# Optimization experiments

Measured on AMD Instinct MI355X. Metric: run time of the kernel, lower is better.

Reference implementation:

```python
import jax, jax.numpy as jnp
import numpy as np

N, E, D, L = 50000, 625000, 128, 7
EPS = 1e-7   # GENConv message epsilon
T = 1.0      # softmax aggregation temperature (learn_t=False)
NUM_ATOM_FEATS, ATOM_VOCAB = 9, 64
NUM_BOND_FEATS, BOND_VOCAB = 3, 8


def setup_inputs() -> dict:
    key = jax.random.key(0)
    ks = jax.random.split(key, 9)
    x = jax.random.randint(ks[0], (N, NUM_ATOM_FEATS), 0, ATOM_VOCAB, dtype=jnp.int32)
    edge_index = jax.random.randint(ks[1], (2, E), 0, N, dtype=jnp.int32)
    edge_attr = jax.random.randint(ks[2], (E, NUM_BOND_FEATS), 0, BOND_VOCAB, dtype=jnp.int32)
    atom_emb = jax.random.normal(ks[3], (NUM_ATOM_FEATS, ATOM_VOCAB, D), dtype=jnp.float32) * 0.1
    bond_emb = jax.random.normal(ks[4], (NUM_BOND_FEATS, BOND_VOCAB, D), dtype=jnp.float32) * 0.1
    W = jax.random.normal(ks[5], (L, D, D), dtype=jnp.float32) / np.sqrt(D).astype(np.float32)
    b = jnp.zeros((L, D), dtype=jnp.float32)
    ln_gamma = jnp.ones((L, D), dtype=jnp.float32)
    ln_beta = jnp.zeros((L, D), dtype=jnp.float32)
    return dict(x=x, edge_index=edge_index, edge_attr=edge_attr,
                atom_emb=atom_emb, bond_emb=bond_emb, W=W, b=b,
                ln_gamma=ln_gamma, ln_beta=ln_beta)


def _layer_norm(h, g, bta):
    mu = jnp.mean(h, axis=-1, keepdims=True)
    var = jnp.var(h, axis=-1, keepdims=True)
    return (h - mu) * jax.lax.rsqrt(var + 1e-5) * g + bta


def _gen_conv(h, src, dst, edge_emb, Wl, bl):
    # GENConv: msg = relu(x_j + e) + eps; softmax aggregation over dst; Linear(x + m)
    msg = jax.nn.relu(h[src] + edge_emb) + EPS                 # [E, D]
    logits = msg * T
    seg_max = jax.ops.segment_max(logits, dst, num_segments=N)  # [N, D]
    seg_max = jnp.where(jnp.isfinite(seg_max), seg_max, 0.0)    # empty segments
    e = jnp.exp(logits - seg_max[dst])                          # [E, D]
    denom = jax.ops.segment_sum(e, dst, num_segments=N)         # [N, D]
    alpha = e / (denom[dst] + 1e-16)
    m = jax.ops.segment_sum(alpha * msg, dst, num_segments=N)   # [N, D]
    return (h + m) @ Wl + bl


def reference(x, edge_index, edge_attr, atom_emb, bond_emb, W, b, ln_gamma, ln_beta):
    src, dst = edge_index[0], edge_index[1]
    # AtomEncoder: sum of per-feature embedding lookups -> [N, D]
    h = jnp.sum(atom_emb[jnp.arange(NUM_ATOM_FEATS)[None, :], x], axis=1)
    # BondEncoder (conv_encode_edge=False: encoded once) -> [E, D]
    edge_emb = jnp.sum(bond_emb[jnp.arange(NUM_BOND_FEATS)[None, :], edge_attr], axis=1)
    # res+ block, dropout=0 (no-op)
    h = _gen_conv(h, src, dst, edge_emb, W[0], b[0])
    for layer in range(1, L):
        h2 = jax.nn.relu(_layer_norm(h, ln_gamma[layer - 1], ln_beta[layer - 1]))
        h = _gen_conv(h2, src, dst, edge_emb, W[layer], b[layer]) + h
    h = _layer_norm(h, ln_gamma[L - 1], ln_beta[L - 1])
    return h
```

## Files before the change

### kernel.cpp

```cpp
#include <hip/hip_runtime.h>
#include <hip/hip_fp16.h>
#include <math.h>


constexpr int D = 128;
constexpr int NA = 9;
constexpr int NB = 3;
constexpr float L2E = 1.4426950408889634f;
constexpr float INV_L2E = 0.6931471805599453f;

using half8  = __attribute__((ext_vector_type(8))) _Float16;
using h2v    = __attribute__((ext_vector_type(2))) _Float16;
using floatx4 = __attribute__((ext_vector_type(4))) float;


__global__ void k_hist(const int* __restrict__ dst, int* __restrict__ deg, int E) {
    int e = blockIdx.x * 256 + threadIdx.x;
    if (e < E) atomicAdd(&deg[dst[e]], 1);
}

__global__ void k_scan_a(const int* __restrict__ deg, int* __restrict__ offs,
                         int* __restrict__ bsum, int N) {
    __shared__ int s[256];
    int i = blockIdx.x * 256 + threadIdx.x;
    int v = (i < N) ? deg[i] : 0;
    s[threadIdx.x] = v;
    __syncthreads();
    for (int d = 1; d < 256; d <<= 1) {
        int add = (threadIdx.x >= d) ? s[threadIdx.x - d] : 0;
        __syncthreads();
        s[threadIdx.x] += add;
        __syncthreads();
    }
    if (i < N) offs[i + 1] = s[threadIdx.x];
    if (threadIdx.x == 255) bsum[blockIdx.x] = s[255];
    if (i == 0) offs[0] = 0;
}

__global__ void k_scan_b(const int* __restrict__ bsum, int* __restrict__ bexc, int nb) {
    __shared__ int s[256];
    int t = threadIdx.x;
    int v = (t < nb) ? bsum[t] : 0;
    s[t] = v;
    __syncthreads();
    for (int d = 1; d < 256; d <<= 1) {
        int add = (t >= d) ? s[t - d] : 0;
        __syncthreads();
        s[t] += add;
        __syncthreads();
    }
    if (t < nb) bexc[t] = s[t] - v;
}

__global__ void k_scan_c_dhist(int* __restrict__ offs, const int* __restrict__ bexc,
                               const int* __restrict__ deg, int* __restrict__ dbin,
                               int N) {
    __shared__ int lb[64];
    int t = threadIdx.x;
    if (t < 64) lb[t] = 0;
    __syncthreads();
    int i = blockIdx.x * 256 + t;
    if (i < N) {
        offs[i + 1] += bexc[blockIdx.x];
        int d = deg[i]; d = d < 63 ? d : 63;
        atomicAdd(&lb[63 - d], 1);
    }
    __syncthreads();
    if (t < 64 && lb[t] > 0) atomicAdd(&dbin[t], lb[t]);
}

__global__ void k_fill(const int* __restrict__ src, const int* __restrict__ dst,
                       const int* __restrict__ attr, const int* __restrict__ offs,
                       int* __restrict__ cur, unsigned* __restrict__ recs1,
                       const int* __restrict__ dbin, int* __restrict__ doff, int E) {
    int e = blockIdx.x * 256 + threadIdx.x;
    if (e < E) {
        int d = dst[e];
        int pos = offs[d] + atomicAdd(&cur[d], 1);
        unsigned cidx = (unsigned)(attr[e * 3] * 64 + attr[e * 3 + 1] * 8 + attr[e * 3 + 2]);
        recs1[pos] = (unsigned)src[e] | (cidx << 17);
    }
    if (blockIdx.x == 0 && threadIdx.x == 0) {
        int acc = 0;
        for (int b = 0; b < 64; ++b) { doff[b] = acc; acc += dbin[b]; }
    }
}


__global__ void k_dfill(const int* __restrict__ deg, const int* __restrict__ doff,
                        int* __restrict__ dcur, int* __restrict__ perm, int N) {
    __shared__ int lc[64], lbase[64];
    int t = threadIdx.x;
    if (t < 64) lc[t] = 0;
    __syncthreads();
    int i = blockIdx.x * 256 + t;
    int b = 0, rank = 0;
    if (i < N) {
        int d = deg[i]; d = d < 63 ? d : 63;
        b = 63 - d;
        rank = atomicAdd(&lc[b], 1);
    }
    __syncthreads();
    if (t < 64 && lc[t] > 0) lbase[t] = atomicAdd(&dcur[t], lc[t]);
    __syncthreads();
    if (i < N) perm[doff[b] + lbase[b] + rank] = i;
}

__global__ void k_comb(const float* __restrict__ bemb, __half* __restrict__ comb16,
                       int* __restrict__ deg, int* __restrict__ cur,
                       int* __restrict__ dbin, int* __restrict__ dcur, int N) {
    int gid = blockIdx.x * 256 + threadIdx.x;
    if (gid < N) { deg[gid] = 0; cur[gid] = 0; }
    if (gid < 64) { dbin[gid] = 0; dcur[gid] = 0; }
    if (gid >= 512 * 32) return;
    int c = gid >> 5, q = gid & 31;
    int a0 = c >> 6, a1 = (c >> 3) & 7, a2 = c & 7;
    float4 v0 = *(const float4*)(bemb + (a0)*D + q * 4);
    float4 v1 = *(const float4*)(bemb + (8 + a1) * D + q * 4);
    float4 v2 = *(const float4*)(bemb + (16 + a2) * D + q * 4);
    __half2* c2 = (__half2*)comb16;
    c2[c * 64 + q * 2]     = __floats2half2_rn(L2E * (v0.x + v1.x + v2.x),
                                               L2E * (v0.y + v1.y + v2.y));
    c2[c * 64 + q * 2 + 1] = __floats2half2_rn(L2E * (v0.z + v1.z + v2.z),
                                               L2E * (v0.w + v1.w + v2.w));
}

__global__ void k_wt(const float* __restrict__ W, __half* __restrict__ Wt16, int total) {
    int o = blockIdx.x * 256 + threadIdx.x;
    if (o >= total) return;
    int l = o >> 14;
    int rem = o & 16383;
    int f = rem >> 7, k = rem & 127;
    Wt16[o] = __float2half_rn(W[(l << 14) + k * 128 + f]);
}


__global__ void k_atom(const int* __restrict__ x, const float* __restrict__ aemb,
                       __half* __restrict__ h16, int N) {
    int wid = (blockIdx.x * blockDim.x + threadIdx.x) >> 6;
    int lane = threadIdx.x & 63;
    if (wid >= N) return;
    const int* xr = x + wid * NA;
    float ax = 0.f, ay = 0.f;
#pragma unroll
    for (int f = 0; f < NA; ++f) {
        int v = xr[f];
        const float2 e = *(const float2*)(aemb + (f * 64 + v) * D + 2 * lane);
        ax += e.x; ay += e.y;
    }
    ((__half2*)h16)[wid * 64 + lane] = __floats2half2_rn(ax * L2E, ay * L2E);
}


__global__ __launch_bounds__(256) void k_agg(const __half* __restrict__ h16,
                      const unsigned* __restrict__ recs1,
                      const int* __restrict__ offs, const __half* __restrict__ comb16,
                      const int* __restrict__ perm,
                      __half* __restrict__ t16, int N) {
    int wid = (blockIdx.x * blockDim.x + threadIdx.x) >> 6;
    int lane = threadIdx.x & 63;
    if (wid >= N) return;
    int nid = perm[wid];
    int su = __builtin_amdgcn_readfirstlane(offs[nid]);
    int eu = __builtin_amdgcn_readfirstlane(offs[nid + 1]);
    h2v hm2 = ((const h2v*)h16)[nid * 64 + lane];
    float hsx = (float)hm2[0], hsy = (float)hm2[1];
    if (su >= eu) {
        ((__half2*)t16)[nid * 64 + lane] =
            __floats2half2_rn(hsx * INV_L2E, hsy * INV_L2E);
        return;
    }
    float Sx = 0.f, Sy = 0.f, Wx = 0.f, Wy = 0.f;

    const h2v* hrow = (const h2v*)h16 + lane;
    const h2v* crow = (const h2v*)comb16 + lane;
    const h2v zero2 = (h2v)(_Float16)0;

    h2v hq[16], cq[16];

    int e0 = su;
    do {
        int lastc = (eu < e0 + 64) ? eu : e0 + 64;
        int last = lastc - 1;
        int ridx = e0 + lane;
        ridx = (ridx < eu - 1) ? ridx : eu - 1;
        unsigned recv = recs1[ridx];

        auto load4 = [&](int base, int slot) {
#pragma unroll
            for (int i = 0; i < 4; ++i) {
                int idx = base + i; idx = (idx < last) ? idx : last;
                unsigned r = __builtin_amdgcn_readlane(recv, idx - e0);
                int sj = (int)(r & 0x1FFFFu);
                int cj = (int)(r >> 17);
                hq[slot * 4 + i] = hrow[sj * 64];
                cq[slot * 4 + i] = crow[cj * 64];
            }
        };
        auto comp4u = [&](int slot) {
#pragma unroll
            for (int i = 0; i < 4; ++i) {
                h2v m = hq[slot * 4 + i] + cq[slot * 4 + i];
                m = __builtin_elementwise_max(m, zero2);
                float u0 = (float)m[0], u1 = (float)m[1];
                float px = __builtin_amdgcn_exp2f(u0);
                float py = __builtin_amdgcn_exp2f(u1);
                Sx += px; Sy += py;
                Wx = fmaf(px, u0, Wx);
                Wy = fmaf(py, u1, Wy);
            }
        };
        auto comp4m = [&](int gb, int slot) {
#pragma unroll
            for (int i = 0; i < 4; ++i) {
                h2v m = hq[slot * 4 + i] + cq[slot * 4 + i];
                m = __builtin_elementwise_max(m, zero2);
                float u0 = (float)m[0], u1 = (float)m[1];
                bool valid = (gb + i) < eu;
                float px = valid ? __builtin_amdgcn_exp2f(u0) : 0.f;
                float py = valid ? __builtin_amdgcn_exp2f(u1) : 0.f;
                Sx += px; Sy += py;
                Wx = fmaf(px, u0, Wx);
                Wy = fmaf(py, u1, Wy);
            }
        };

        load4(e0, 0);
        if (e0 + 4  < lastc) load4(e0 + 4, 1);
        if (e0 + 8  < lastc) load4(e0 + 8, 2);
        if (e0 + 12 < lastc) load4(e0 + 12, 3);

        int e = e0;
        for (; e + 16 < lastc; e += 16) {
            comp4u(0); comp4u(1); comp4u(2); comp4u(3);
            load4(e + 16, 0); load4(e + 20, 1); load4(e + 24, 2); load4(e + 28, 3);
        }
        comp4m(e, 0);
        if (e + 4  < lastc) comp4m(e + 4, 1);
        if (e + 8  < lastc) comp4m(e + 8, 2);
        if (e + 12 < lastc) comp4m(e + 12, 3);

        e0 = lastc;
    } while (e0 < eu);

    float tx = (hsx + Wx / (Sx + 1e-16f)) * INV_L2E;
    float ty = (hsy + Wy / (Sy + 1e-16f)) * INV_L2E;
    ((__half2*)t16)[nid * 64 + lane] = __floats2half2_rn(tx, ty);
}


template <int MODE>
__global__ __launch_bounds__(256) void k_gemm(const __half* __restrict__ A16,
                                              const __half* __restrict__ Wt16,
                                              const float* __restrict__ bl,
                                              const __half* __restrict__ res16,
                                              __half* __restrict__ hres16,
                                              const float* __restrict__ g,
                                              const float* __restrict__ bta,
                                              __half* __restrict__ h16,
                                              float* __restrict__ out,
                                              int N, int useRes) {
    __shared__ float2 sm[2][2][16];
    int lane = threadIdx.x & 63;
    int wave = threadIdx.x >> 6;
    int grp = wave >> 1, half = wave & 1;
    int quad = lane >> 4, col = lane & 15;
    int node = blockIdx.x * 32 + grp * 16 + col;
    bool nok = node < N;
    int nc = nok ? node : N - 1;

    const __half* arow = A16 + (size_t)nc * 128;
    half8 bfrag[4];
#pragma unroll
    for (int ks = 0; ks < 4; ++ks)
        bfrag[ks] = *(const half8*)(arow + ks * 32 + quad * 8);

    uint2 rr[4];
    if (useRes) {
#pragma unroll
        for (int ft2 = 0; ft2 < 4; ++ft2) {
            int f0 = (half * 4 + ft2) * 16 + quad * 4;
            rr[ft2] = *(const uint2*)(res16 + (size_t)nc * 128 + f0);
        }
    }

    floatx4 acc[4];
#pragma unroll
    for (int ft2 = 0; ft2 < 4; ++ft2) acc[ft2] = (floatx4){0.f, 0.f, 0.f, 0.f};

#pragma unroll
    for (int ft2 = 0; ft2 < 4; ++ft2) {
        const __half* wrow = Wt16 + (size_t)((half * 4 + ft2) * 16 + col) * 128;
#pragma unroll
        for (int ks = 0; ks < 4; ++ks) {
            half8 afrag = *(const half8*)(wrow + ks * 32 + quad * 8);
            acc[ft2] = __builtin_amdgcn_mfma_f32_16x16x32_f16(afrag, bfrag[ks],
                                                              acc[ft2], 0, 0, 0);
        }
    }

    float s = 0.f, ss = 0.f;
#pragma unroll
    for (int ft2 = 0; ft2 < 4; ++ft2) {
        int f0 = (half * 4 + ft2) * 16 + quad * 4;
        float4 bb = *(const float4*)(bl + f0);
        float o0 = acc[ft2][0] + bb.x, o1 = acc[ft2][1] + bb.y;
        float o2 = acc[ft2][2] + bb.z, o3 = acc[ft2][3] + bb.w;
        if (useRes) {
            __half2 r01 = *(__half2*)&rr[ft2].x, r23 = *(__half2*)&rr[ft2].y;
            o0 += __low2float(r01); o1 += __high2float(r01);
            o2 += __low2float(r23); o3 += __high2float(r23);
        }
        acc[ft2][0] = o0; acc[ft2][1] = o1; acc[ft2][2] = o2; acc[ft2][3] = o3;
        s += (o0 + o1) + (o2 + o3);
        ss += fmaf(o0, o0, o1 * o1) + fmaf(o2, o2, o3 * o3);
        if (MODE == 0 && nok) {
            __half2 h01 = __floats2half2_rn(o0, o1);
            __half2 h23 = __floats2half2_rn(o2, o3);
            uint2 pk = make_uint2(*(unsigned*)&h01, *(unsigned*)&h23);
            *(uint2*)(hres16 + (size_t)node * 128 + f0) = pk;
        }
    }
    s += __shfl_xor(s, 16, 64);  ss += __shfl_xor(ss, 16, 64);
    s += __shfl_xor(s, 32, 64);  ss += __shfl_xor(ss, 32, 64);
    if (quad == 0) sm[grp][half][col] = make_float2(s, ss);
    __syncthreads();
    float2 oth = sm[grp][half ^ 1][col];
    float st = s + oth.x, sst = ss + oth.y;
    float mu = st * (1.f / 128.f);
    float var = sst * (1.f / 128.f) - mu * mu;
    float rs = rsqrtf(var + 1e-5f);

#pragma unroll
    for (int ft2 = 0; ft2 < 4; ++ft2) {
        int f0 = (half * 4 + ft2) * 16 + quad * 4;
        float4 gg = *(const float4*)(g + f0);
        float4 bt = *(const float4*)(bta + f0);
        float l0 = (acc[ft2][0] - mu) * rs * gg.x + bt.x;
        float l1 = (acc[ft2][1] - mu) * rs * gg.y + bt.y;
        float l2 = (acc[ft2][2] - mu) * rs * gg.z + bt.z;
        float l3 = (acc[ft2][3] - mu) * rs * gg.w + bt.w;
        if (MODE == 0) {
            l0 = fmaxf(l0, 0.f); l1 = fmaxf(l1, 0.f);
            l2 = fmaxf(l2, 0.f); l3 = fmaxf(l3, 0.f);
            if (nok) {
                __half2 h01 = __floats2half2_rn(l0 * L2E, l1 * L2E);
                __half2 h23 = __floats2half2_rn(l2 * L2E, l3 * L2E);
                uint2 pk = make_uint2(*(unsigned*)&h01, *(unsigned*)&h23);
                *(uint2*)(h16 + (size_t)node * 128 + f0) = pk;
            }
        } else {
            if (nok)
                *(float4*)(out + (size_t)node * 128 + f0) =
                    make_float4(l0, l1, l2, l3);
        }
    }
}


extern "C" void kernel_launch(void* const* d_in, const int* in_sizes, int n_in,
                              void* d_out, int out_size, void* d_ws, size_t ws_size,
                              hipStream_t stream) {
    const int*   x    = (const int*)d_in[0];
    const int*   ei   = (const int*)d_in[1];
    const int*   attr = (const int*)d_in[2];
    const float* aemb = (const float*)d_in[3];
    const float* bemb = (const float*)d_in[4];
    const float* Wf   = (const float*)d_in[5];
    const float* bf   = (const float*)d_in[6];
    const float* gam  = (const float*)d_in[7];
    const float* bet  = (const float*)d_in[8];
    float* out = (float*)d_out;

    const int N = in_sizes[0] / NA;
    const int E = in_sizes[1] / 2;
    const int L = in_sizes[5] / (D * D);

    char* ws = (char*)d_ws;
    size_t o = 0;
    auto carve = [&](size_t bytes) -> void* {
        void* p = (void*)(ws + o);
        o += (bytes + 255) & ~(size_t)255;
        return p;
    };
    __half* hres16 = (__half*)carve((size_t)N * D * 2);
    __half* h16    = (__half*)carve((size_t)N * D * 2);
    __half* t16    = (__half*)carve((size_t)N * D * 2);
    unsigned* recs1 = (unsigned*)carve((size_t)E * 4);
    __half* comb16 = (__half*)carve(512 * D * 2);
    __half* Wt16   = (__half*)carve((size_t)L * D * D * 2);
    int*    deg    = (int*)carve((size_t)N * 4);
    int*    cur    = (int*)carve((size_t)N * 4);
    int*    offs   = (int*)carve((size_t)(N + 1) * 4);
    int*    perm   = (int*)carve((size_t)N * 4);
    int*    dbin   = (int*)carve(256);
    int*    doff   = (int*)carve(256);
    int*    dcur   = (int*)carve(256);
    int*    bsum   = (int*)carve(4096);
    int*    bexc   = (int*)carve(4096);

    const int* src = ei;
    const int* dst = ei + E;

    int ebl = (E + 255) / 256;
    int nbl = (N + 255) / 256;

    k_comb<<<nbl, 256, 0, stream>>>(bemb, comb16, deg, cur, dbin, dcur, N);
    int wtot = L * D * D;
    k_wt<<<(wtot + 255) / 256, 256, 0, stream>>>(Wf, Wt16, wtot);
    k_hist<<<ebl, 256, 0, stream>>>(dst, deg, E);
    k_scan_a<<<nbl, 256, 0, stream>>>(deg, offs, bsum, N);
    k_scan_b<<<1, 256, 0, stream>>>(bsum, bexc, nbl);
    k_scan_c_dhist<<<nbl, 256, 0, stream>>>(offs, bexc, deg, dbin, N);
    k_fill<<<ebl, 256, 0, stream>>>(src, dst, attr, offs, cur, recs1, dbin, doff, E);
    k_dfill<<<nbl, 256, 0, stream>>>(deg, doff, dcur, perm, N);

    int wbl = (N * 64 + 255) / 256;
    k_atom<<<wbl, 256, 0, stream>>>(x, aemb, h16, N);

    int gbl = (N + 31) / 32;
    for (int l = 0; l < L; ++l) {
        k_agg<<<wbl, 256, 0, stream>>>(h16, recs1, offs, comb16, perm, t16, N);
        if (l == L - 1) {
            k_gemm<1><<<gbl, 256, 0, stream>>>(t16, Wt16 + l * D * D, bf + l * D,
                                               hres16, hres16,
                                               gam + l * D, bet + l * D, h16, out,
                                               N, 1);
        } else {
            k_gemm<0><<<gbl, 256, 0, stream>>>(t16, Wt16 + l * D * D, bf + l * D,
                                               hres16, hres16,
                                               gam + l * D, bet + l * D, h16, out,
                                               N, l > 0 ? 1 : 0);
        }
    }
}
```

Before: 585.2 us.

## Process four degree-sorted nodes per wave with packed node metadata

Aggregation now assigns four nodes (consecutive in the degree-sorted order) to each wavefront instead of one. A packed int4 metadata array (edge start, edge end, node id) replaces the separate perm and offs lookups, and the first chunk of edge records for all four nodes is prefetched up front. The compute/load interleave in the inner loop is also reordered so each slot's loads are issued right after its compute. This amortises per-node launch and lookup latency and exposes more memory-level parallelism for low-degree nodes, at the cost of serialising four nodes within a wave and adding an extra padded metadata buffer.

After: 590.2 us. No clear change (+0.8%).

```diff
diff --git a/kernel.cpp b/kernel.cpp
--- a/kernel.cpp
+++ b/kernel.cpp
@@ -88,7 +88,8 @@
 
 
 __global__ void k_dfill(const int* __restrict__ deg, const int* __restrict__ doff,
-                        int* __restrict__ dcur, int* __restrict__ perm, int N) {
+                        int* __restrict__ dcur, const int* __restrict__ offs,
+                        int4* __restrict__ meta, int N) {
     __shared__ int lc[64], lbase[64];
     int t = threadIdx.x;
     if (t < 64) lc[t] = 0;
@@ -103,15 +104,18 @@
     __syncthreads();
     if (t < 64 && lc[t] > 0) lbase[t] = atomicAdd(&dcur[t], lc[t]);
     __syncthreads();
-    if (i < N) perm[doff[b] + lbase[b] + rank] = i;
+    if (i < N)
+        meta[doff[b] + lbase[b] + rank] = make_int4(offs[i], offs[i + 1], i, 0);
 }
 
 __global__ void k_comb(const float* __restrict__ bemb, __half* __restrict__ comb16,
                        int* __restrict__ deg, int* __restrict__ cur,
-                       int* __restrict__ dbin, int* __restrict__ dcur, int N) {
+                       int* __restrict__ dbin, int* __restrict__ dcur,
+                       int4* __restrict__ meta, int N, int N4) {
     int gid = blockIdx.x * 256 + threadIdx.x;
     if (gid < N) { deg[gid] = 0; cur[gid] = 0; }
     if (gid < 64) { dbin[gid] = 0; dcur[gid] = 0; }
+    if (gid >= N && gid < N4) meta[gid] = make_int4(0, 0, -1, 0);
     if (gid >= 512 * 32) return;
     int c = gid >> 5, q = gid & 31;
     int a0 = c >> 6, a1 = (c >> 3) & 7, a2 = c & 7;
@@ -154,98 +158,120 @@
 
 __global__ __launch_bounds__(256) void k_agg(const __half* __restrict__ h16,
                       const unsigned* __restrict__ recs1,
-                      const int* __restrict__ offs, const __half* __restrict__ comb16,
-                      const int* __restrict__ perm,
+                      const int4* __restrict__ meta,
+                      const __half* __restrict__ comb16,
                       __half* __restrict__ t16, int N) {
-    int wid = (blockIdx.x * blockDim.x + threadIdx.x) >> 6;
+    int w = (blockIdx.x * blockDim.x + threadIdx.x) >> 6;
     int lane = threadIdx.x & 63;
-    if (wid >= N) return;
-    int nid = perm[wid];
-    int su = __builtin_amdgcn_readfirstlane(offs[nid]);
-    int eu = __builtin_amdgcn_readfirstlane(offs[nid + 1]);
-    h2v hm2 = ((const h2v*)h16)[nid * 64 + lane];
-    float hsx = (float)hm2[0], hsy = (float)hm2[1];
-    if (su >= eu) {
-        ((__half2*)t16)[nid * 64 + lane] =
-            __floats2half2_rn(hsx * INV_L2E, hsy * INV_L2E);
-        return;
-    }
-    float Sx = 0.f, Sy = 0.f, Wx = 0.f, Wy = 0.f;
+    int base = w * 4;
+    if (base >= N) return;
 
     const h2v* hrow = (const h2v*)h16 + lane;
     const h2v* crow = (const h2v*)comb16 + lane;
     const h2v zero2 = (h2v)(_Float16)0;
 
-    h2v hq[16], cq[16];
-
-    int e0 = su;
-    do {
-        int lastc = (eu < e0 + 64) ? eu : e0 + 64;
-        int last = lastc - 1;
-        int ridx = e0 + lane;
-        ridx = (ridx < eu - 1) ? ridx : eu - 1;
-        unsigned recv = recs1[ridx];
-
-        auto load4 = [&](int base, int slot) {
-#pragma unroll
-            for (int i = 0; i < 4; ++i) {
-                int idx = base + i; idx = (idx < last) ? idx : last;
-                unsigned r = __builtin_amdgcn_readlane(recv, idx - e0);
-                int sj = (int)(r & 0x1FFFFu);
-                int cj = (int)(r >> 17);
-                hq[slot * 4 + i] = hrow[sj * 64];
-                cq[slot * 4 + i] = crow[cj * 64];
+    int4 m0 = meta[base], m1 = meta[base + 1], m2 = meta[base + 2], m3 = meta[base + 3];
+    int su0 = __builtin_amdgcn_readfirstlane(m0.x), eu0 = __builtin_amdgcn_readfirstlane(m0.y), nid0 = __builtin_amdgcn_readfirstlane(m0.z);
+    int su1 = __builtin_amdgcn_readfirstlane(m1.x), eu1 = __builtin_amdgcn_readfirstlane(m1.y), nid1 = __builtin_amdgcn_readfirstlane(m1.z);
+    int su2 = __builtin_amdgcn_readfirstlane(m2.x), eu2 = __builtin_amdgcn_readfirstlane(m2.y), nid2 = __builtin_amdgcn_readfirstlane(m2.z);
+    int su3 = __builtin_amdgcn_readfirstlane(m3.x), eu3 = __builtin_amdgcn_readfirstlane(m3.y), nid3 = __builtin_amdgcn_readfirstlane(m3.z);
+
+    unsigned rv0 = 0, rv1 = 0, rv2 = 0, rv3 = 0;
+    if (su0 < eu0) { int ri = su0 + lane; ri = (ri < eu0 - 1) ? ri : eu0 - 1; rv0 = recs1[ri]; }
+    if (su1 < eu1) { int ri = su1 + lane; ri = (ri < eu1 - 1) ? ri : eu1 - 1; rv1 = recs1[ri]; }
+    if (su2 < eu2) { int ri = su2 + lane; ri = (ri < eu2 - 1) ? ri : eu2 - 1; rv2 = recs1[ri]; }
+    if (su3 < eu3) { int ri = su3 + lane; ri = (ri < eu3 - 1) ? ri : eu3 - 1; rv3 = recs1[ri]; }
+
+    auto process = [&](int su, int eu, int nid, unsigned recv) {
+        if (nid < 0) return;
+        h2v hm2 = hrow[nid * 64];
+        if (su >= eu) {
+            ((__half2*)t16)[nid * 64 + lane] = __floats2half2_rn(
+                (float)hm2[0] * INV_L2E, (float)hm2[1] * INV_L2E);
+            return;
+        }
+        float Sx = 0.f, Sy = 0.f, Wx = 0.f, Wy = 0.f;
+        h2v hq[16], cq[16];
+        int e0 = su;
+        bool first = true;
+        do {
+            int lastc = (eu < e0 + 64) ? eu : e0 + 64;
+            int last = lastc - 1;
+            if (!first) {
+                int ri = e0 + lane;
+                ri = (ri < eu - 1) ? ri : eu - 1;
+                recv = recs1[ri];
             }
-        };
-        auto comp4u = [&](int slot) {
-#pragma unroll
-            for (int i = 0; i < 4; ++i) {
-                h2v m = hq[slot * 4 + i] + cq[slot * 4 + i];
-                m = __builtin_elementwise_max(m, zero2);
-                float u0 = (float)m[0], u1 = (float)m[1];
-                float px = __builtin_amdgcn_exp2f(u0);
-                float py = __builtin_amdgcn_exp2f(u1);
-                Sx += px; Sy += py;
-                Wx = fmaf(px, u0, Wx);
-                Wy = fmaf(py, u1, Wy);
+            first = false;
+
+            auto load4 = [&](int b2, int slot) {
+#pragma unroll
+                for (int i = 0; i < 4; ++i) {
+                    int idx = b2 + i; idx = (idx < last) ? idx : last;
+                    unsigned r = __builtin_amdgcn_readlane(recv, idx - e0);
+                    int sj = (int)(r & 0x1FFFFu);
+                    int cj = (int)(r >> 17);
+                    hq[slot * 4 + i] = hrow[sj * 64];
+                    cq[slot * 4 + i] = crow[cj * 64];
+                }
+            };
+            auto comp4u = [&](int slot) {
+#pragma unroll
+                for (int i = 0; i < 4; ++i) {
+                    h2v m = hq[slot * 4 + i] + cq[slot * 4 + i];
+                    m = __builtin_elementwise_max(m, zero2);
+                    float u0 = (float)m[0], u1 = (float)m[1];
+                    float px = __builtin_amdgcn_exp2f(u0);
+                    float py = __builtin_amdgcn_exp2f(u1);
+                    Sx += px; Sy += py;
+                    Wx = fmaf(px, u0, Wx);
+                    Wy = fmaf(py, u1, Wy);
+                }
+            };
+            auto comp4m = [&](int gb, int slot) {
+#pragma unroll
+                for (int i = 0; i < 4; ++i) {
+                    h2v m = hq[slot * 4 + i] + cq[slot * 4 + i];
+                    m = __builtin_elementwise_max(m, zero2);
+                    float u0 = (float)m[0], u1 = (float)m[1];
+                    bool valid = (gb + i) < eu;
+                    float px = valid ? __builtin_amdgcn_exp2f(u0) : 0.f;
+                    float py = valid ? __builtin_amdgcn_exp2f(u1) : 0.f;
+                    Sx += px; Sy += py;
+                    Wx = fmaf(px, u0, Wx);
+                    Wy = fmaf(py, u1, Wy);
+                }
+            };
+
+            load4(e0, 0);
+            if (e0 + 4  < lastc) load4(e0 + 4, 1);
+            if (e0 + 8  < lastc) load4(e0 + 8, 2);
+            if (e0 + 12 < lastc) load4(e0 + 12, 3);
+
+            int e = e0;
+            for (; e + 16 < lastc; e += 16) {
+                comp4u(0); load4(e + 16, 0);
+                comp4u(1); load4(e + 20, 1);
+                comp4u(2); load4(e + 24, 2);
+                comp4u(3); load4(e + 28, 3);
             }
-        };
-        auto comp4m = [&](int gb, int slot) {
-#pragma unroll
-            for (int i = 0; i < 4; ++i) {
-                h2v m = hq[slot * 4 + i] + cq[slot * 4 + i];
-                m = __builtin_elementwise_max(m, zero2);
-                float u0 = (float)m[0], u1 = (float)m[1];
-                bool valid = (gb + i) < eu;
-                float px = valid ? __builtin_amdgcn_exp2f(u0) : 0.f;
-                float py = valid ? __builtin_amdgcn_exp2f(u1) : 0.f;
-                Sx += px; Sy += py;
-                Wx = fmaf(px, u0, Wx);
-                Wy = fmaf(py, u1, Wy);
-            }
-        };
-
-        load4(e0, 0);
-        if (e0 + 4  < lastc) load4(e0 + 4, 1);
-        if (e0 + 8  < lastc) load4(e0 + 8, 2);
-        if (e0 + 12 < lastc) load4(e0 + 12, 3);
-
-        int e = e0;
-        for (; e + 16 < lastc; e += 16) {
-            comp4u(0); comp4u(1); comp4u(2); comp4u(3);
-            load4(e + 16, 0); load4(e + 20, 1); load4(e + 24, 2); load4(e + 28, 3);
-        }
-        comp4m(e, 0);
-        if (e + 4  < lastc) comp4m(e + 4, 1);
-        if (e + 8  < lastc) comp4m(e + 8, 2);
-        if (e + 12 < lastc) comp4m(e + 12, 3);
-
-        e0 = lastc;
-    } while (e0 < eu);
-
-    float tx = (hsx + Wx / (Sx + 1e-16f)) * INV_L2E;
-    float ty = (hsy + Wy / (Sy + 1e-16f)) * INV_L2E;
-    ((__half2*)t16)[nid * 64 + lane] = __floats2half2_rn(tx, ty);
+            comp4m(e, 0);
+            if (e + 4  < lastc) comp4m(e + 4, 1);
+            if (e + 8  < lastc) comp4m(e + 8, 2);
+            if (e + 12 < lastc) comp4m(e + 12, 3);
+
+            e0 = lastc;
+        } while (e0 < eu);
+
+        float tx = ((float)hm2[0] + Wx / (Sx + 1e-16f)) * INV_L2E;
+        float ty = ((float)hm2[1] + Wy / (Sy + 1e-16f)) * INV_L2E;
+        ((__half2*)t16)[nid * 64 + lane] = __floats2half2_rn(tx, ty);
+    };
+
+    process(su0, eu0, nid0, rv0);
+    process(su1, eu1, nid1, rv1);
+    process(su2, eu2, nid2, rv2);
+    process(su3, eu3, nid3, rv3);
 }
 
 
@@ -375,6 +401,7 @@
     const int N = in_sizes[0] / NA;
     const int E = in_sizes[1] / 2;
     const int L = in_sizes[5] / (D * D);
+    const int N4 = (N + 3) & ~3;
 
     char* ws = (char*)d_ws;
     size_t o = 0;
@@ -392,7 +419,7 @@
     int*    deg    = (int*)carve((size_t)N * 4);
     int*    cur    = (int*)carve((size_t)N * 4);
     int*    offs   = (int*)carve((size_t)(N + 1) * 4);
-    int*    perm   = (int*)carve((size_t)N * 4);
+    int4*   meta   = (int4*)carve((size_t)N4 * 16);
     int*    dbin   = (int*)carve(256);
     int*    doff   = (int*)carve(256);
     int*    dcur   = (int*)carve(256);
@@ -405,7 +432,7 @@
     int ebl = (E + 255) / 256;
     int nbl = (N + 255) / 256;
 
-    k_comb<<<nbl, 256, 0, stream>>>(bemb, comb16, deg, cur, dbin, dcur, N);
+    k_comb<<<nbl, 256, 0, stream>>>(bemb, comb16, deg, cur, dbin, dcur, meta, N, N4);
     int wtot = L * D * D;
     k_wt<<<(wtot + 255) / 256, 256, 0, stream>>>(Wf, Wt16, wtot);
     k_hist<<<ebl, 256, 0, stream>>>(dst, deg, E);
@@ -413,14 +440,16 @@
     k_scan_b<<<1, 256, 0, stream>>>(bsum, bexc, nbl);
     k_scan_c_dhist<<<nbl, 256, 0, stream>>>(offs, bexc, deg, dbin, N);
     k_fill<<<ebl, 256, 0, stream>>>(src, dst, attr, offs, cur, recs1, dbin, doff, E);
-    k_dfill<<<nbl, 256, 0, stream>>>(deg, doff, dcur, perm, N);
+    k_dfill<<<nbl, 256, 0, stream>>>(deg, doff, dcur, offs, meta, N);
 
     int wbl = (N * 64 + 255) / 256;
     k_atom<<<wbl, 256, 0, stream>>>(x, aemb, h16, N);
 
+    int nwv = N4 / 4;
+    int abl = (nwv * 64 + 255) / 256;
     int gbl = (N + 31) / 32;
     for (int l = 0; l < L; ++l) {
-        k_agg<<<wbl, 256, 0, stream>>>(h16, recs1, offs, comb16, perm, t16, N);
+        k_agg<<<abl, 256, 0, stream>>>(h16, recs1, meta, comb16, t16, N);
         if (l == L - 1) {
             k_gemm<1><<<gbl, 256, 0, stream>>>(t16, Wt16 + l * D * D, bf + l * D,
                                                hres16, hres16,
```
